# Optimization experiments

Hardware: AMD Instinct MI355X
Metric: run time of the kernel (lower is better)

The kernel has to match this reference:

```python
import jax, jax.numpy as jnp
import numpy as np

N = 30000          # nodes
E = 480000         # directed edges (avg degree 16)
F_IN = 376         # num_features (hard-coded in module)
HID = 512          # nhid (hard-coded)
NEG_SLOPE = 0.2    # PyG GATConv default negative_slope


def _lin(k, fi, fo):
    return (jax.random.normal(k, (fi, fo), jnp.float32) / np.sqrt(fi)).astype(jnp.float32)


def setup_inputs() -> dict:
    key = jax.random.key(0)
    ks = jax.random.split(key, 16)
    d = {}
    d["x"] = jax.random.normal(ks[0], (N, F_IN), jnp.float32)
    d["edge_index"] = jax.random.randint(ks[1], (2, E), 0, N)
    d["edge_weight"] = jax.random.uniform(ks[2], (E,), jnp.float32)
    # GCNConv(376,512) and GCNConv(512,512)
    d["W1"] = _lin(ks[3], F_IN, HID); d["b1"] = jnp.zeros((HID,), jnp.float32)
    d["W2"] = _lin(ks[4], HID, HID);  d["b2"] = jnp.zeros((HID,), jnp.float32)
    # SAGEConv(512,512): lin_l on aggregated neighbors, lin_r on root
    d["sage_Wl"] = _lin(ks[5], HID, HID)
    d["sage_Wr"] = _lin(ks[6], HID, HID)
    d["sage_b"] = jnp.zeros((HID,), jnp.float32)
    # GATConv(1536, 1, heads=4, concat=False)
    d["gat1_W"] = _lin(ks[7], 3 * HID, 4)
    d["gat1_a_src"] = jax.random.normal(ks[8], (4,), jnp.float32) * 0.1
    d["gat1_a_dst"] = jax.random.normal(ks[9], (4,), jnp.float32) * 0.1
    d["gat1_b"] = jnp.zeros((1,), jnp.float32)
    # GATConv(1536, 1, heads=16, concat=False)
    d["gat2_W"] = _lin(ks[10], 3 * HID, 16)
    d["gat2_a_src"] = jax.random.normal(ks[11], (16,), jnp.float32) * 0.1
    d["gat2_a_dst"] = jax.random.normal(ks[12], (16,), jnp.float32) * 0.1
    d["gat2_b"] = jnp.zeros((1,), jnp.float32)
    return d


def gcn_conv(x, src, dst, ew, W, b, n):
    # PyG GCNConv: add self-loops (weight 1), symmetric normalization
    loop = jnp.arange(n)
    s = jnp.concatenate([src, loop])
    t = jnp.concatenate([dst, loop])
    w = jnp.concatenate([ew, jnp.ones((n,), ew.dtype)])
    deg = jax.ops.segment_sum(w, t, num_segments=n)
    dinv = jnp.where(deg > 0, jax.lax.rsqrt(deg), 0.0)
    norm = dinv[s] * w * dinv[t]                       # [E+N]
    h = x @ W                                           # [N, out]
    out = jax.ops.segment_sum(norm[:, None] * h[s], t, num_segments=n)
    return out + b


def sage_conv(x, src, dst, Wl, Wr, b, n):
    # PyG SAGEConv: mean neighbor aggregation + root transform
    sums = jax.ops.segment_sum(x[src], dst, num_segments=n)
    cnt = jax.ops.segment_sum(jnp.ones((src.shape[0],), x.dtype), dst, num_segments=n)
    mean = sums / jnp.maximum(cnt, 1.0)[:, None]
    return mean @ Wl + x @ Wr + b


def gat_conv(x, src, dst, W, a_src, a_dst, b, n):
    # PyG GATConv (out_channels=1, concat=False -> mean over heads), self-loops added
    loop = jnp.arange(n)
    s = jnp.concatenate([src, loop])
    t = jnp.concatenate([dst, loop])
    h = x @ W                                           # [N, heads] (C=1)
    e = jax.nn.leaky_relu(h[s] * a_src + h[t] * a_dst, NEG_SLOPE)  # [E+N, heads]
    m = jax.ops.segment_max(e, t, num_segments=n)       # stable segment softmax
    ex = jnp.exp(e - m[t])
    den = jax.ops.segment_sum(ex, t, num_segments=n)
    alpha = ex / den[t]
    out = jax.ops.segment_sum(alpha * h[s], t, num_segments=n)     # [N, heads]
    return out.mean(axis=1, keepdims=True) + b          # [N, 1]


def reference(x, edge_index, edge_weight, W1, b1, W2, b2,
              sage_Wl, sage_Wr, sage_b,
              gat1_W, gat1_a_src, gat1_a_dst, gat1_b,
              gat2_W, gat2_a_src, gat2_a_dst, gat2_b):
    n = x.shape[0]
    src, dst = edge_index[0], edge_index[1]
    x1 = jax.nn.relu(gcn_conv(x, src, dst, edge_weight, W1, b1, n))
    x2 = jax.nn.relu(gcn_conv(x1, src, dst, edge_weight, W2, b2, n))
    x3 = jax.nn.relu(sage_conv(x1, src, dst, sage_Wl, sage_Wr, sage_b, n))
    dense_features = jnp.concatenate([x1, x2, x3], axis=1)  # [N, 1536]
    a1 = gat_conv(dense_features, src, dst, gat1_W, gat1_a_src, gat1_a_dst, gat1_b, n)
    a2 = gat_conv(dense_features, src, dst, gat2_W, gat2_a_src, gat2_a_dst, gat2_b, n)
    x_out = jnp.ravel((a1 + a2) * 0.5)                  # [N]
    return x_out, dense_features
```

## Files before the change

kernel.cpp:

```cpp
#include <hip/hip_runtime.h>
#include <hip/hip_bf16.h>
#include <stdint.h>

#define N_NODES 30000
#define M_PAD   30080
#define N_EDGES 480000
#define F_IN 376
#define K1   384
#define HID 512
#define DENSE_F 1536
#define NHEADS 20
#define HG_LD 32

typedef __bf16 bf16_t;
typedef bf16_t bf16x8 __attribute__((ext_vector_type(8)));
typedef float  f32x4  __attribute__((ext_vector_type(4)));

#define S1 (512 * K1)
#define S2 (512 * 512)
#define S3 (512 * 1024)
#define S4 (128 * DENSE_F)
#define PW_ELEMS (S1 + S2 + S3 + S4 + NHEADS)

#define EB_BLOCKS ((N_EDGES + 255) / 256)
#define CX_BLOCKS ((M_PAD * K1) / 256)
#define PW_BLOCKS ((PW_ELEMS + 255) / 256)
#define PRO_BLOCKS (EB_BLOCKS + CX_BLOCKS + PW_BLOCKS)

__global__ __launch_bounds__(256) void prologue(
    const int* __restrict__ dst, const float* __restrict__ ew,
    float* __restrict__ deg, int* __restrict__ cnt,
    const float* __restrict__ x, bf16_t* __restrict__ xb,
    const float* __restrict__ W1, const float* __restrict__ W2,
    const float* __restrict__ Wl, const float* __restrict__ Wr,
    const float* __restrict__ g1W, const float* __restrict__ g2W,
    const float* __restrict__ a1s, const float* __restrict__ a1d,
    const float* __restrict__ a2s, const float* __restrict__ a2d,
    bf16_t* __restrict__ W1t, bf16_t* __restrict__ W2t,
    bf16_t* __restrict__ Bst, bf16_t* __restrict__ Wgt,
    float* __restrict__ asrc, float* __restrict__ adst)
{
    int b = blockIdx.x;
    if (b < EB_BLOCKS) {
        int e = b * 256 + threadIdx.x;
        if (e >= N_EDGES) return;
        int t = dst[e];
        atomicAdd(&deg[t], ew[e]);
        atomicAdd(&cnt[t], 1);
    } else if (b < EB_BLOCKS + CX_BLOCKS) {
        int tid = (b - EB_BLOCKS) * 256 + threadIdx.x;
        int r = tid / K1, c = tid - r * K1;
        float v = (r < N_NODES && c < F_IN) ? x[r * F_IN + c] : 0.f;
        xb[tid] = (bf16_t)v;
    } else {
        int tid = (b - EB_BLOCKS - CX_BLOCKS) * 256 + threadIdx.x;
        if (tid < S1) {
            int n = tid / K1, k = tid - n * K1;
            W1t[tid] = (bf16_t)((k < F_IN) ? W1[k * HID + n] : 0.f);
        } else if (tid < S1 + S2) {
            int t = tid - S1;
            int n = t >> 9, k = t & 511;
            W2t[t] = (bf16_t)W2[k * HID + n];
        } else if (tid < S1 + S2 + S3) {
            int t = tid - S1 - S2;
            int n = t >> 10, k = t & 1023;
            Bst[t] = (bf16_t)((k < HID) ? Wl[k * HID + n] : Wr[(k - HID) * HID + n]);
        } else if (tid < S1 + S2 + S3 + S4) {
            int t = tid - S1 - S2 - S3;
            int n = t / DENSE_F, k = t - n * DENSE_F;
            float v = (n < 4) ? g1W[k * 4 + n] : (n < NHEADS) ? g2W[k * 16 + (n - 4)] : 0.f;
            Wgt[t] = (bf16_t)v;
        } else if (tid < S1 + S2 + S3 + S4 + NHEADS) {
            int hh = tid - S1 - S2 - S3 - S4;
            asrc[hh] = (hh < 4) ? a1s[hh] : a2s[hh - 4];
            adst[hh] = (hh < 4) ? a1d[hh] : a2d[hh - 4];
        }
    }
}

#define SEG 30
__global__ __launch_bounds__(1024) void scan_rowptr_fast(
    const int* __restrict__ cnt, int* __restrict__ rowptr, int* __restrict__ woff,
    float* __restrict__ deg, float* __restrict__ dinv)
{
    int t = threadIdx.x;
    int base = t * SEG;
    int v[SEG];
    int sum = 0;
#pragma unroll
    for (int j = 0; j < SEG; ++j) {
        int i = base + j;
        int c = (i < N_NODES) ? cnt[i] : 0;
        v[j] = c;
        sum += c;
        if (i < N_NODES) {
            float d = deg[i] + 1.0f;
            deg[i] = d;
            dinv[i] = rsqrtf(d);
        }
    }
    int lane = t & 63;
    int wid = t >> 6;
    int s = sum;
#pragma unroll
    for (int off = 1; off < 64; off <<= 1) {
        int u = __shfl_up(s, off);
        if (lane >= off) s += u;
    }
    __shared__ int wsum[16];
    if (lane == 63) wsum[wid] = s;
    __syncthreads();
    if (t < 16) {
        int ws = wsum[t];
#pragma unroll
        for (int off = 1; off < 16; off <<= 1) {
            int u = __shfl_up(ws, off);
            if (t >= off) ws += u;
        }
        wsum[t] = ws;
    }
    __syncthreads();
    int carry = (wid > 0) ? wsum[wid - 1] : 0;
    int excl = carry + s - sum;
#pragma unroll
    for (int j = 0; j < SEG; ++j) {
        int i = base + j;
        if (i < N_NODES) { rowptr[i] = excl; woff[i] = excl; }
        excl += v[j];
    }
    if (t == 1023) rowptr[N_NODES] = excl;
}

__global__ __launch_bounds__(256) void scatter_csr(
    const int* __restrict__ src, const int* __restrict__ dst,
    const float* __restrict__ ew, int* __restrict__ woff,
    int* __restrict__ col, float* __restrict__ wcsr)
{
    int e = blockIdx.x * 256 + threadIdx.x;
    if (e >= N_EDGES) return;
    int t = dst[e];
    int p = atomicAdd(&woff[t], 1);
    col[p] = src[e];
    wcsr[p] = ew[e];
}

#define TILE_E (128 * 32)
__device__ __forceinline__ void gemm_body(
    const bf16_t* __restrict__ A1, int lda1, int ksplit,
    const bf16_t* __restrict__ A2, int lda2,
    const bf16_t* __restrict__ Bt, int ldb,
    float* __restrict__ C, bf16_t* __restrict__ Cb, long ldc, int K,
    const float* __restrict__ bias, int ncols,
    int n0, long r0, bf16_t* As, bf16_t* Bs)
{
    const int tid = threadIdx.x;
    const int wid = tid >> 6, lane = tid & 63;
    const int li = lane & 15, kq = lane >> 4;
    const int wm = (wid >> 1) * 64, wn = (wid & 1) * 64;

    f32x4 acc[4][4] = {};

    const int s0 = wid * 64 + lane;
    const int s1 = 256 + s0;
    const int am0 = s0 >> 2, ak0 = (s0 & 3) ^ ((am0 >> 1) & 3);
    const int am1 = s1 >> 2, ak1 = (s1 & 3) ^ ((am1 >> 1) & 3);
    const int swz = (li >> 1) & 3;

    auto stage = [&](int buf, int k0) {
        const bf16_t* Ab; int lda;
        if (k0 < ksplit) { Ab = A1 + k0;            lda = lda1; }
        else             { Ab = A2 + (k0 - ksplit); lda = lda2; }
        bf16_t* Asb = As + buf * TILE_E;
        bf16_t* Bsb = Bs + buf * TILE_E;
        __builtin_amdgcn_global_load_lds(
            (const __attribute__((address_space(1))) void*)(Ab + (r0 + am0) * (long)lda + ak0 * 8),
            (__attribute__((address_space(3))) void*)(Asb + (wid * 64) * 8), 16, 0, 0);
        __builtin_amdgcn_global_load_lds(
            (const __attribute__((address_space(1))) void*)(Ab + (r0 + am1) * (long)lda + ak1 * 8),
            (__attribute__((address_space(3))) void*)(Asb + (256 + wid * 64) * 8), 16, 0, 0);
        __builtin_amdgcn_global_load_lds(
            (const __attribute__((address_space(1))) void*)(Bt + (n0 + am0) * (long)ldb + k0 + ak0 * 8),
            (__attribute__((address_space(3))) void*)(Bsb + (wid * 64) * 8), 16, 0, 0);
        __builtin_amdgcn_global_load_lds(
            (const __attribute__((address_space(1))) void*)(Bt + (n0 + am1) * (long)ldb + k0 + ak1 * 8),
            (__attribute__((address_space(3))) void*)(Bsb + (256 + wid * 64) * 8), 16, 0, 0);
    };

    const int nsteps = K >> 5;
    stage(0, 0);
    __syncthreads();

    int cur = 0;
    for (int s = 0; s < nsteps; ++s) {
        if (s + 1 < nsteps) stage(cur ^ 1, (s + 1) << 5);

        const bf16_t* Asb = As + cur * TILE_E;
        const bf16_t* Bsb = Bs + cur * TILE_E;
        bf16x8 a[4], b[4];
#pragma unroll
        for (int f = 0; f < 4; ++f) {
            int m = wm + f * 16 + li;
            a[f] = *(const bf16x8*)(Asb + m * 32 + ((kq ^ swz) * 8));
            int n = wn + f * 16 + li;
            b[f] = *(const bf16x8*)(Bsb + n * 32 + ((kq ^ swz) * 8));
        }
#pragma unroll
        for (int fm = 0; fm < 4; ++fm)
#pragma unroll
            for (int fn = 0; fn < 4; ++fn)
                acc[fm][fn] = __builtin_amdgcn_mfma_f32_16x16x32_bf16(
                    a[fm], b[fn], acc[fm][fn], 0, 0, 0);
        __syncthreads();
        cur ^= 1;
    }

#pragma unroll
    for (int fm = 0; fm < 4; ++fm) {
#pragma unroll
        for (int r = 0; r < 4; ++r) {
            long row = r0 + wm + fm * 16 + kq * 4 + r;
            if (row >= N_NODES) continue;
#pragma unroll
            for (int fn = 0; fn < 4; ++fn) {
                int colg = n0 + wn + fn * 16 + li;
                if (colg >= ncols) continue;
                float v = acc[fm][fn][r];
                if (bias) v = fmaxf(v + bias[colg], 0.f);
                if (C)  C[row * ldc + colg]  = v;
                if (Cb) Cb[row * ldc + colg] = (bf16_t)v;
            }
        }
    }
}

__global__ __launch_bounds__(256) void gemm_bf16(
    const bf16_t* __restrict__ A1, int lda1, int ksplit,
    const bf16_t* __restrict__ A2, int lda2,
    const bf16_t* __restrict__ Bt, int ldb,
    float* __restrict__ C, bf16_t* __restrict__ Cb, long ldc, int K,
    const float* __restrict__ bias, int ncols)
{
    __shared__ bf16_t As[2 * TILE_E];
    __shared__ bf16_t Bs[2 * TILE_E];
    gemm_body(A1, lda1, ksplit, A2, lda2, Bt, ldb, C, Cb, ldc, K, bias, ncols,
              blockIdx.x * 128, (long)blockIdx.y * 128, As, Bs);
}

__global__ __launch_bounds__(256) void gemm_bf16_dual(
    const bf16_t* __restrict__ A1a, int lda1a, int ksplita,
    const bf16_t* __restrict__ A2a, int lda2a,
    const bf16_t* __restrict__ Bta, int ldba,
    float* __restrict__ Ca, bf16_t* __restrict__ Cba, long ldca, int Ka,
    const float* __restrict__ biasa, int ncolsa,
    const bf16_t* __restrict__ A1b, int lda1b, int ksplitb,
    const bf16_t* __restrict__ A2b, int lda2b,
    const bf16_t* __restrict__ Btb, int ldbb,
    float* __restrict__ Cb2, bf16_t* __restrict__ Cbb, long ldcb, int Kb,
    const float* __restrict__ biasb, int ncolsb)
{
    __shared__ bf16_t As[2 * TILE_E];
    __shared__ bf16_t Bs[2 * TILE_E];
    long r0 = (long)blockIdx.y * 128;
    if (blockIdx.x < 4) {
        gemm_body(A1a, lda1a, ksplita, A2a, lda2a, Bta, ldba, Ca, Cba, ldca, Ka,
                  biasa, ncolsa, blockIdx.x * 128, r0, As, Bs);
    } else {
        gemm_body(A1b, lda1b, ksplitb, A2b, lda2b, Btb, ldbb, Cb2, Cbb, ldcb, Kb,
                  biasb, ncolsb, (blockIdx.x - 4) * 128, r0, As, Bs);
    }
}

__global__ __launch_bounds__(256) void agg_x(
    const bf16_t* __restrict__ xb, const int* __restrict__ rowptr,
    const int* __restrict__ col, const float* __restrict__ wcsr,
    const float* __restrict__ dinv, const float* __restrict__ deg,
    bf16_t* __restrict__ aggx)
{
    int i = blockIdx.x * 4 + (threadIdx.x >> 6);
    int lane = threadIdx.x & 63;
    int c = lane * 8;
    bool act = (c < K1);
    float di = dinv[i];
    float selfw = 1.0f / deg[i];
    float acc0[8] = {}, acc1[8] = {};
    if (act) {
        bf16x8 sv = *(const bf16x8*)(xb + (long)i * K1 + c);
#pragma unroll
        for (int j = 0; j < 8; ++j) acc0[j] = selfw * (float)sv[j];
    }
    int e = rowptr[i], e1 = rowptr[i + 1];
    for (; e + 3 < e1; e += 4) {
        int sA = col[e], sB = col[e + 1], sC = col[e + 2], sD = col[e + 3];
        float wA = dinv[sA] * wcsr[e]     * di;
        float wB = dinv[sB] * wcsr[e + 1] * di;
        float wC = dinv[sC] * wcsr[e + 2] * di;
        float wD = dinv[sD] * wcsr[e + 3] * di;
        if (act) {
            bf16x8 vA = *(const bf16x8*)(xb + (long)sA * K1 + c);
            bf16x8 vB = *(const bf16x8*)(xb + (long)sB * K1 + c);
            bf16x8 vC = *(const bf16x8*)(xb + (long)sC * K1 + c);
            bf16x8 vD = *(const bf16x8*)(xb + (long)sD * K1 + c);
#pragma unroll
            for (int j = 0; j < 8; ++j) {
                acc0[j] = fmaf(wA, (float)vA[j], acc0[j]);
                acc1[j] = fmaf(wB, (float)vB[j], acc1[j]);
                acc0[j] = fmaf(wC, (float)vC[j], acc0[j]);
                acc1[j] = fmaf(wD, (float)vD[j], acc1[j]);
            }
        }
    }
    for (; e < e1; ++e) {
        int sA = col[e];
        float wA = dinv[sA] * wcsr[e] * di;
        if (act) {
            bf16x8 vA = *(const bf16x8*)(xb + (long)sA * K1 + c);
#pragma unroll
            for (int j = 0; j < 8; ++j) acc0[j] = fmaf(wA, (float)vA[j], acc0[j]);
        }
    }
    if (act) {
        bf16x8 ob;
#pragma unroll
        for (int j = 0; j < 8; ++j) ob[j] = (bf16_t)(acc0[j] + acc1[j]);
        *reinterpret_cast<bf16x8*>(aggx + (long)i * K1 + c) = ob;
    }
}

__global__ __launch_bounds__(256) void agg_x1(
    const bf16_t* __restrict__ x1b ,
    const int* __restrict__ rowptr, const int* __restrict__ col,
    const float* __restrict__ wcsr, const float* __restrict__ dinv,
    const float* __restrict__ deg, const int* __restrict__ cnt,
    bf16_t* __restrict__ gbf, bf16_t* __restrict__ meanb)
{
    int i = blockIdx.x * 4 + (threadIdx.x >> 6);
    int lane = threadIdx.x & 63;
    int c = lane * 8;
    float di = dinv[i];
    float selfw = 1.0f / deg[i];
    bf16x8 sv = *(const bf16x8*)(x1b + (long)i * DENSE_F + c);
    float g0[8], g1[8], m0[8], m1[8];
#pragma unroll
    for (int j = 0; j < 8; ++j) {
        g0[j] = selfw * (float)sv[j];
        g1[j] = 0.f; m0[j] = 0.f; m1[j] = 0.f;
    }
    int e = rowptr[i], e1 = rowptr[i + 1];
    for (; e + 3 < e1; e += 4) {
        int sA = col[e], sB = col[e + 1], sC = col[e + 2], sD = col[e + 3];
        float wA = dinv[sA] * wcsr[e]     * di;
        float wB = dinv[sB] * wcsr[e + 1] * di;
        float wC = dinv[sC] * wcsr[e + 2] * di;
        float wD = dinv[sD] * wcsr[e + 3] * di;
        bf16x8 vA = *(const bf16x8*)(x1b + (long)sA * DENSE_F + c);
        bf16x8 vB = *(const bf16x8*)(x1b + (long)sB * DENSE_F + c);
        bf16x8 vC = *(const bf16x8*)(x1b + (long)sC * DENSE_F + c);
        bf16x8 vD = *(const bf16x8*)(x1b + (long)sD * DENSE_F + c);
#pragma unroll
        for (int j = 0; j < 8; ++j) {
            float fA = (float)vA[j], fB = (float)vB[j];
            float fC = (float)vC[j], fD = (float)vD[j];
            g0[j] = fmaf(wA, fA, g0[j]);
            g1[j] = fmaf(wB, fB, g1[j]);
            g0[j] = fmaf(wC, fC, g0[j]);
            g1[j] = fmaf(wD, fD, g1[j]);
            m0[j] += fA + fC;
            m1[j] += fB + fD;
        }
    }
    for (; e < e1; ++e) {
        int sA = col[e];
        float wA = dinv[sA] * wcsr[e] * di;
        bf16x8 vA = *(const bf16x8*)(x1b + (long)sA * DENSE_F + c);
#pragma unroll
        for (int j = 0; j < 8; ++j) {
            float fA = (float)vA[j];
            g0[j] = fmaf(wA, fA, g0[j]);
            m0[j] += fA;
        }
    }
    float inv = 1.0f / fmaxf((float)cnt[i], 1.0f);
    bf16x8 og, om;
#pragma unroll
    for (int j = 0; j < 8; ++j) {
        og[j] = (bf16_t)(g0[j] + g1[j]);
        om[j] = (bf16_t)((m0[j] + m1[j]) * inv);
    }
    *reinterpret_cast<bf16x8*>(gbf   + (long)i * HID + c) = og;
    *reinterpret_cast<bf16x8*>(meanb + (long)i * HID + c) = om;
}

__global__ __launch_bounds__(256) void gat_agg(
    const float* __restrict__ hgat, const int* __restrict__ rowptr,
    const int* __restrict__ col, const float* __restrict__ asrc,
    const float* __restrict__ adst, const float* __restrict__ b1p,
    const float* __restrict__ b2p, float* __restrict__ xout)
{
    int i = blockIdx.x * 4 + (threadIdx.x >> 6);
    int lane = threadIdx.x & 63;
    int h = (lane < NHEADS) ? lane : 0;
    float hg_i = hgat[(long)i * HG_LD + h];
    float as = asrc[h], ad = adst[h];
    float adhg = ad * hg_i;
    float ev = hg_i * as + adhg;
    ev = ev > 0.f ? ev : 0.2f * ev;
    float ex = __expf(ev);
    float den0 = ex, og0 = ex * hg_i, den1 = 0.f, og1 = 0.f;
    int e = rowptr[i], e1 = rowptr[i + 1];
    for (; e + 3 < e1; e += 4) {
        int sA = col[e], sB = col[e + 1], sC = col[e + 2], sD = col[e + 3];
        float hA = hgat[(long)sA * HG_LD + h];
        float hB = hgat[(long)sB * HG_LD + h];
        float hC = hgat[(long)sC * HG_LD + h];
        float hD = hgat[(long)sD * HG_LD + h];
        float tA = fmaf(hA, as, adhg); tA = tA > 0.f ? tA : 0.2f * tA;
        float tB = fmaf(hB, as, adhg); tB = tB > 0.f ? tB : 0.2f * tB;
        float tC = fmaf(hC, as, adhg); tC = tC > 0.f ? tC : 0.2f * tC;
        float tD = fmaf(hD, as, adhg); tD = tD > 0.f ? tD : 0.2f * tD;
        float xA = __expf(tA), xB = __expf(tB);
        float xC = __expf(tC), xD = __expf(tD);
        den0 += xA; og0 = fmaf(xA, hA, og0);
        den1 += xB; og1 = fmaf(xB, hB, og1);
        den0 += xC; og0 = fmaf(xC, hC, og0);
        den1 += xD; og1 = fmaf(xD, hD, og1);
    }
    for (; e < e1; ++e) {
        int sA = col[e];
        float hA = hgat[(long)sA * HG_LD + h];
        float tA = fmaf(hA, as, adhg); tA = tA > 0.f ? tA : 0.2f * tA;
        float xA = __expf(tA);
        den0 += xA; og0 = fmaf(xA, hA, og0);
    }
    float out = (lane < NHEADS) ? (og0 + og1) / (den0 + den1) : 0.f;
    float s4 = out + __shfl_xor(out, 1);
    s4 += __shfl_xor(s4, 2);
    float g0 = __shfl(s4, 0);
    float g1 = __shfl(s4, 4);
    float g2 = __shfl(s4, 8);
    float g3 = __shfl(s4, 12);
    float g4 = __shfl(s4, 16);
    if (lane == 0) {
        float a1 = g0 * 0.25f + b1p[0];
        float a2 = (g1 + g2 + g3 + g4) * 0.0625f + b2p[0];
        xout[i] = 0.5f * (a1 + a2);
    }
}

extern "C" void kernel_launch(void* const* d_in, const int* in_sizes, int n_in,
                              void* d_out, int out_size, void* d_ws, size_t ws_size,
                              hipStream_t stream) {
    (void)in_sizes; (void)n_in; (void)out_size; (void)ws_size;
    const float* x    = (const float*)d_in[0];
    const int*   ei   = (const int*)d_in[1];
    const float* ew   = (const float*)d_in[2];
    const float* W1   = (const float*)d_in[3];
    const float* b1   = (const float*)d_in[4];
    const float* W2   = (const float*)d_in[5];
    const float* b2   = (const float*)d_in[6];
    const float* sWl  = (const float*)d_in[7];
    const float* sWr  = (const float*)d_in[8];
    const float* sb   = (const float*)d_in[9];
    const float* g1W  = (const float*)d_in[10];
    const float* g1as = (const float*)d_in[11];
    const float* g1ad = (const float*)d_in[12];
    const float* g1b  = (const float*)d_in[13];
    const float* g2W  = (const float*)d_in[14];
    const float* g2as = (const float*)d_in[15];
    const float* g2ad = (const float*)d_in[16];
    const float* g2b  = (const float*)d_in[17];

    const int* src = ei;
    const int* dst = ei + N_EDGES;

    float* xout  = (float*)d_out;
    float* dense = xout + N_NODES;

    size_t off = 0;
    auto alloc = [&](size_t nbytes) -> void* {
        void* p = (char*)d_ws + off;
        off += (nbytes + 255) & ~(size_t)255;
        return p;
    };
    bf16_t* dense_bf = (bf16_t*)alloc((size_t)M_PAD * DENSE_F * 2);
    bf16_t* x_bf     = (bf16_t*)alloc((size_t)M_PAD * K1 * 2);
    bf16_t* aggx_bf  = (bf16_t*)alloc((size_t)M_PAD * K1 * 2);
    bf16_t* g_bf     = (bf16_t*)alloc((size_t)M_PAD * HID * 2);
    bf16_t* mean_bf  = (bf16_t*)alloc((size_t)M_PAD * HID * 2);
    float*  hgat     = (float*)alloc((size_t)M_PAD * HG_LD * 4);
    bf16_t* W1t      = (bf16_t*)alloc((size_t)512 * K1 * 2);
    bf16_t* W2t      = (bf16_t*)alloc((size_t)512 * 512 * 2);
    bf16_t* Bst      = (bf16_t*)alloc((size_t)512 * 1024 * 2);
    bf16_t* Wgt      = (bf16_t*)alloc((size_t)128 * DENSE_F * 2);
    float*  deg      = (float*)alloc((size_t)N_NODES * 4);
    float*  dinv     = (float*)alloc((size_t)N_NODES * 4);
    float*  asrc     = (float*)alloc(32 * 4);
    float*  adst     = (float*)alloc(32 * 4);
    int*    cnt      = (int*)alloc((size_t)N_NODES * 4);
    int*    rowp     = (int*)alloc((size_t)(N_NODES + 1) * 4);
    int*    woff     = (int*)alloc((size_t)N_NODES * 4);
    int*    colx     = (int*)alloc((size_t)N_EDGES * 4);
    float*  wcsr     = (float*)alloc((size_t)N_EDGES * 4);

    const int EB = EB_BLOCKS;

    hipMemsetAsync(deg, 0, (size_t)N_NODES * 4, stream);
    hipMemsetAsync(cnt, 0, (size_t)N_NODES * 4, stream);

    prologue<<<PRO_BLOCKS, 256, 0, stream>>>(
        dst, ew, deg, cnt, x, x_bf,
        W1, W2, sWl, sWr, g1W, g2W, g1as, g1ad, g2as, g2ad,
        W1t, W2t, Bst, Wgt, asrc, adst);
    scan_rowptr_fast<<<1, 1024, 0, stream>>>(cnt, rowp, woff, deg, dinv);
    scatter_csr<<<EB, 256, 0, stream>>>(src, dst, ew, woff, colx, wcsr);

    const dim3 gB(256);
    const dim3 g512(HID / 128, M_PAD / 128);
    const dim3 gdual(8, M_PAD / 128);
    const dim3 g128(1, M_PAD / 128);

    agg_x<<<N_NODES / 4, 256, 0, stream>>>(x_bf, rowp, colx, wcsr, dinv, deg, aggx_bf);
    gemm_bf16<<<g512, gB, 0, stream>>>(aggx_bf, K1, K1, aggx_bf, K1, W1t, K1,
                                       dense, dense_bf, DENSE_F, K1, b1, 512);

    agg_x1<<<N_NODES / 4, 256, 0, stream>>>(dense_bf, rowp, colx, wcsr, dinv, deg, cnt,
                                            g_bf, mean_bf);
    gemm_bf16_dual<<<gdual, gB, 0, stream>>>(
        g_bf, HID, HID, g_bf, HID, W2t, HID,
        dense + HID, dense_bf + HID, DENSE_F, HID, b2, 512,
        mean_bf, HID, HID, dense_bf, DENSE_F, Bst, 1024,
        dense + 2 * HID, dense_bf + 2 * HID, DENSE_F, 1024, sb, 512);

    gemm_bf16<<<g128, gB, 0, stream>>>(dense_bf, DENSE_F, DENSE_F, dense_bf, DENSE_F,
                                       Wgt, DENSE_F, hgat, nullptr, HG_LD,
                                       DENSE_F, nullptr, HG_LD);
    gat_agg<<<N_NODES / 4, 256, 0, stream>>>(hgat, rowp, colx, asrc, adst, g1b, g2b, xout);
}
```

Measured before the change: 818.8 us.

## Triple-buffer GEMM LDS pipeline and remap workgroups across XCDs

The GEMM main loop moves from a double-buffered LDS scheme with a full __syncthreads per step to a three-stage ring. Loads are issued two steps ahead, and explicit vmcnt waits plus raw s_barrier let memory traffic overlap the MFMA work. Launches become 1D, and each block's index is remapped so consecutive tiles land on the same XCD, which should improve L2 reuse of shared A/B panels. LDS use grows by half per block, which may reduce occupancy. The hand-written waitcnt counts also depend on each thread issuing exactly four loads per stage.

Result: faster. 763.5 us (-6.8%).

```diff
diff --git a/kernel.cpp b/kernel.cpp
--- a/kernel.cpp
+++ b/kernel.cpp
@@ -144,14 +144,24 @@
     wcsr[p] = ew[e];
 }
 
-#define TILE_E (128 * 32)
+__device__ __forceinline__ void xcd_remap(int nwg, int gx, int& bx, int& by)
+{
+    int d = blockIdx.x;
+    int xcd = d & 7, pos = d >> 3;
+    int q = nwg >> 3, r = nwg & 7;
+    int l = (xcd < r ? xcd * (q + 1) : r * (q + 1) + (xcd - r) * q) + pos;
+    bx = l % gx;
+    by = l / gx;
+}
+
+#define BUF_E (128 * 32)
 __device__ __forceinline__ void gemm_body(
     const bf16_t* __restrict__ A1, int lda1, int ksplit,
     const bf16_t* __restrict__ A2, int lda2,
     const bf16_t* __restrict__ Bt, int ldb,
     float* __restrict__ C, bf16_t* __restrict__ Cb, long ldc, int K,
     const float* __restrict__ bias, int ncols,
-    int n0, long r0, bf16_t* As, bf16_t* Bs)
+    int n0, long r0, bf16_t* smem)
 {
     const int tid = threadIdx.x;
     const int wid = tid >> 6, lane = tid & 63;
@@ -170,8 +180,8 @@
         const bf16_t* Ab; int lda;
         if (k0 < ksplit) { Ab = A1 + k0;            lda = lda1; }
         else             { Ab = A2 + (k0 - ksplit); lda = lda2; }
-        bf16_t* Asb = As + buf * TILE_E;
-        bf16_t* Bsb = Bs + buf * TILE_E;
+        bf16_t* Asb = smem + buf * (2 * BUF_E);
+        bf16_t* Bsb = Asb + BUF_E;
         __builtin_amdgcn_global_load_lds(
             (const __attribute__((address_space(1))) void*)(Ab + (r0 + am0) * (long)lda + ak0 * 8),
             (__attribute__((address_space(3))) void*)(Asb + (wid * 64) * 8), 16, 0, 0);
@@ -188,14 +198,23 @@
 
     const int nsteps = K >> 5;
     stage(0, 0);
-    __syncthreads();
-
-    int cur = 0;
+    stage(1, 32);
+
+    int cur = 0, nx2 = 2;
     for (int s = 0; s < nsteps; ++s) {
-        if (s + 1 < nsteps) stage(cur ^ 1, (s + 1) << 5);
-
-        const bf16_t* Asb = As + cur * TILE_E;
-        const bf16_t* Bsb = Bs + cur * TILE_E;
+        if (s + 2 < nsteps) {
+            stage(nx2, (s + 2) << 5);
+            asm volatile("s_waitcnt vmcnt(8)" ::: "memory");
+        } else if (s + 2 == nsteps) {
+            asm volatile("s_waitcnt vmcnt(4)" ::: "memory");
+        } else {
+            asm volatile("s_waitcnt vmcnt(0)" ::: "memory");
+        }
+        __builtin_amdgcn_s_barrier();
+        __builtin_amdgcn_sched_barrier(0);
+
+        const bf16_t* Asb = smem + cur * (2 * BUF_E);
+        const bf16_t* Bsb = Asb + BUF_E;
         bf16x8 a[4], b[4];
 #pragma unroll
         for (int f = 0; f < 4; ++f) {
@@ -210,8 +229,13 @@
             for (int fn = 0; fn < 4; ++fn)
                 acc[fm][fn] = __builtin_amdgcn_mfma_f32_16x16x32_bf16(
                     a[fm], b[fn], acc[fm][fn], 0, 0, 0);
-        __syncthreads();
-        cur ^= 1;
+
+        __builtin_amdgcn_sched_barrier(0);
+        __builtin_amdgcn_s_barrier();
+        __builtin_amdgcn_sched_barrier(0);
+
+        cur = (cur == 2) ? 0 : cur + 1;
+        nx2 = (nx2 == 2) ? 0 : nx2 + 1;
     }
 
 #pragma unroll
@@ -238,12 +262,13 @@
     const bf16_t* __restrict__ A2, int lda2,
     const bf16_t* __restrict__ Bt, int ldb,
     float* __restrict__ C, bf16_t* __restrict__ Cb, long ldc, int K,
-    const float* __restrict__ bias, int ncols)
-{
-    __shared__ bf16_t As[2 * TILE_E];
-    __shared__ bf16_t Bs[2 * TILE_E];
+    const float* __restrict__ bias, int ncols, int gx)
+{
+    __shared__ bf16_t smem[3 * 2 * BUF_E];
+    int bx, by;
+    xcd_remap((int)gridDim.x, gx, bx, by);
     gemm_body(A1, lda1, ksplit, A2, lda2, Bt, ldb, C, Cb, ldc, K, bias, ncols,
-              blockIdx.x * 128, (long)blockIdx.y * 128, As, Bs);
+              bx * 128, (long)by * 128, smem);
 }
 
 __global__ __launch_bounds__(256) void gemm_bf16_dual(
@@ -258,15 +283,16 @@
     float* __restrict__ Cb2, bf16_t* __restrict__ Cbb, long ldcb, int Kb,
     const float* __restrict__ biasb, int ncolsb)
 {
-    __shared__ bf16_t As[2 * TILE_E];
-    __shared__ bf16_t Bs[2 * TILE_E];
-    long r0 = (long)blockIdx.y * 128;
-    if (blockIdx.x < 4) {
+    __shared__ bf16_t smem[3 * 2 * BUF_E];
+    int bx, by;
+    xcd_remap((int)gridDim.x, 8, bx, by);
+    long r0 = (long)by * 128;
+    if (bx < 4) {
         gemm_body(A1a, lda1a, ksplita, A2a, lda2a, Bta, ldba, Ca, Cba, ldca, Ka,
-                  biasa, ncolsa, blockIdx.x * 128, r0, As, Bs);
+                  biasa, ncolsa, bx * 128, r0, smem);
     } else {
         gemm_body(A1b, lda1b, ksplitb, A2b, lda2b, Btb, ldbb, Cb2, Cbb, ldcb, Kb,
-                  biasb, ncolsb, (blockIdx.x - 4) * 128, r0, As, Bs);
+                  biasb, ncolsb, (bx - 4) * 128, r0, smem);
     }
 }
 
@@ -514,24 +540,22 @@
     scatter_csr<<<EB, 256, 0, stream>>>(src, dst, ew, woff, colx, wcsr);
 
     const dim3 gB(256);
-    const dim3 g512(HID / 128, M_PAD / 128);
-    const dim3 gdual(8, M_PAD / 128);
-    const dim3 g128(1, M_PAD / 128);
+    const int NT = M_PAD / 128;
 
     agg_x<<<N_NODES / 4, 256, 0, stream>>>(x_bf, rowp, colx, wcsr, dinv, deg, aggx_bf);
-    gemm_bf16<<<g512, gB, 0, stream>>>(aggx_bf, K1, K1, aggx_bf, K1, W1t, K1,
-                                       dense, dense_bf, DENSE_F, K1, b1, 512);
+    gemm_bf16<<<4 * NT, gB, 0, stream>>>(aggx_bf, K1, K1, aggx_bf, K1, W1t, K1,
+                                         dense, dense_bf, DENSE_F, K1, b1, 512, 4);
 
     agg_x1<<<N_NODES / 4, 256, 0, stream>>>(dense_bf, rowp, colx, wcsr, dinv, deg, cnt,
                                             g_bf, mean_bf);
-    gemm_bf16_dual<<<gdual, gB, 0, stream>>>(
+    gemm_bf16_dual<<<8 * NT, gB, 0, stream>>>(
         g_bf, HID, HID, g_bf, HID, W2t, HID,
         dense + HID, dense_bf + HID, DENSE_F, HID, b2, 512,
         mean_bf, HID, HID, dense_bf, DENSE_F, Bst, 1024,
         dense + 2 * HID, dense_bf + 2 * HID, DENSE_F, 1024, sb, 512);
 
-    gemm_bf16<<<g128, gB, 0, stream>>>(dense_bf, DENSE_F, DENSE_F, dense_bf, DENSE_F,
-                                       Wgt, DENSE_F, hgat, nullptr, HG_LD,
-                                       DENSE_F, nullptr, HG_LD);
+    gemm_bf16<<<1 * NT, gB, 0, stream>>>(dense_bf, DENSE_F, DENSE_F, dense_bf, DENSE_F,
+                                         Wgt, DENSE_F, hgat, nullptr, HG_LD,
+                                         DENSE_F, nullptr, HG_LD, 1);
     gat_agg<<<N_NODES / 4, 256, 0, stream>>>(hgat, rowp, colx, asrc, adst, g1b, g2b, xout);
 }
```
